# Performance work log

Measured on AMD Instinct MI355X. Metric: run time of the kernel, lower is better.

The kernel has to match this reference:

```python
import jax, jax.numpy as jnp
import numpy as np

N, E, B = 20000, 100000, 16
U_SZ, U_RED = 4096, 256
EDGE_H, EDGE_OUT = 1024, 512
NODE_H = 512
X_DIM, EA_DIM = 9, 1


def _lin(key, fan_out, fan_in):
    kw, kb = jax.random.split(key)
    s = 1.0 / np.sqrt(fan_in)
    w = jax.random.uniform(kw, (fan_out, fan_in), jnp.float32, -s, s)
    b = jax.random.uniform(kb, (fan_out,), jnp.float32, -s, s)
    return w, b


def setup_inputs() -> dict:
    key = jax.random.key(0)
    ks = jax.random.split(key, 16)
    inp = {}
    inp["x"] = jax.random.normal(ks[0], (N, X_DIM), jnp.float32)
    inp["edge_index"] = jax.random.randint(ks[1], (2, E), 0, N, jnp.int64)
    inp["edge_attr"] = jax.random.normal(ks[2], (E, EA_DIM), jnp.float32)
    inp["u"] = jax.random.normal(ks[3], (B, U_SZ), jnp.float32)
    inp["batch"] = jnp.sort(jax.random.randint(ks[4], (N,), 0, B, jnp.int64))
    # select_dim_reduction: Linear(4096, 256)
    inp["w_sel"], inp["b_sel"] = _lin(ks[5], U_RED, U_SZ)
    # edge MLP: 275 -> 1024 -> 1024 -> 1024 -> 1024 -> 512
    e_in = EA_DIM + 2 * X_DIM + U_RED  # 275
    inp["ew0"], inp["eb0"] = _lin(ks[6], EDGE_H, e_in)
    inp["ew1"], inp["eb1"] = _lin(ks[7], EDGE_H, EDGE_H)
    inp["ew2"], inp["eb2"] = _lin(ks[8], EDGE_H, EDGE_H)
    inp["ew3"], inp["eb3"] = _lin(ks[9], EDGE_H, EDGE_H)
    inp["ew4"], inp["eb4"] = _lin(ks[10], EDGE_OUT, EDGE_H)
    # node_mlp_1: (9+512) -> 512 -> 512 (relu after each)
    inp["nw0"], inp["nb0"] = _lin(ks[11], NODE_H, X_DIM + EDGE_OUT)
    inp["nw1"], inp["nb1"] = _lin(ks[12], NODE_H, NODE_H)
    # node_mlp_2: (9+512+256) -> 512 -> 1
    inp["mw0"], inp["mb0"] = _lin(ks[13], NODE_H, X_DIM + NODE_H + U_RED)
    inp["mw1"], inp["mb1"] = _lin(ks[14], 1, NODE_H)
    return inp


def reference(x, edge_index, edge_attr, u, batch,
              w_sel, b_sel,
              ew0, eb0, ew1, eb1, ew2, eb2, ew3, eb3, ew4, eb4,
              nw0, nb0, nw1, nb1, mw0, mb0, mw1, mb1):
    row, col = edge_index[0], edge_index[1]
    u_r = u @ w_sel.T + b_sel                       # [B, 256]
    eb_idx = batch[row]                             # edge -> graph
    # EdgeModel: cat([src, dest, edge_attr, u[batch]]) -> MLP
    e_in = jnp.concatenate([x[row], x[col], edge_attr, u_r[eb_idx]], axis=1)  # [E,275]
    h = jax.nn.relu(e_in @ ew0.T + eb0)
    h = jax.nn.relu(h @ ew1.T + eb1)
    h = jax.nn.relu(h @ ew2.T + eb2)
    h = jax.nn.relu(h @ ew3.T + eb3)
    edge_out = h @ ew4.T + eb4                      # [E, 512]
    # NodeModel: gather x[col], edge MLP, scatter_mean onto row
    n_in = jnp.concatenate([x[col], edge_out], axis=1)  # [E, 521]
    h = jax.nn.relu(n_in @ nw0.T + nb0)
    h = jax.nn.relu(h @ nw1.T + nb1)                # [E, 512]
    seg_sum = jax.ops.segment_sum(h, row, num_segments=x.shape[0])
    cnt = jax.ops.segment_sum(jnp.ones((h.shape[0],), h.dtype), row, num_segments=x.shape[0])
    agg = seg_sum / jnp.maximum(cnt, 1.0)[:, None]  # scatter_mean
    m_in = jnp.concatenate([x, agg, u_r[batch]], axis=1)  # [N, 777]
    h2 = jax.nn.relu(m_in @ mw0.T + mb0)
    out = h2 @ mw1.T + mb1                          # [N, 1]
    return jnp.squeeze(out)
```

## Files before the change

kernel.cpp:

```cpp
#include <hip/hip_runtime.h>


#define NN 20000
#define EE 100000
#define BB 16

typedef _Float16 f16x8 __attribute__((ext_vector_type(8)));
typedef _Float16 f16x4 __attribute__((ext_vector_type(4)));
typedef float f32x4 __attribute__((ext_vector_type(4)));

__device__ __forceinline__ int clampi(int v, int hi) {
    return v < 0 ? 0 : (v >= hi ? hi - 1 : v);
}

__device__ __forceinline__ void gld_lds16(const void* g, void* l) {
    __builtin_amdgcn_global_load_lds(
        (const __attribute__((address_space(1))) unsigned int*)g,
        (__attribute__((address_space(3))) unsigned int*)l, 16, 0, 0);
}

template <int MODE>
__global__ __launch_bounds__(256, 4) void gemm_blk(
    const _Float16* __restrict__ A,
    const _Float16* __restrict__ Wt,
    int KT, int KTs,
    const float* __restrict__ bias, int ldbias, const int* __restrict__ gbid,
    void* __restrict__ C, int KTo, int ktOff,
    int ldc,
    const int* __restrict__ srow, float* __restrict__ aux,
    int M, int relu)
{
    __shared__ char smem[32768];
    _Float16* As = (_Float16*)smem;
    _Float16* Bs = As + 8192;

    const int tid  = threadIdx.x;
    const int lane = tid & 63;
    const int wid  = tid >> 6;
    const int wm = (wid & 1) << 6;
    const int wn = (wid >> 1) << 6;

    const int nb = gridDim.x;
    const int MT = gridDim.y;
    int f = blockIdx.y * nb + blockIdx.x;
    const int MT8 = MT & ~7;
    int p, c;
    if (f < MT8 * nb) {
        c = (f >> 3) % nb;
        p = (f & 7) + 8 * ((f >> 3) / nb);
    } else {
        int g = f - MT8 * nb;
        p = MT8 + g / nb;
        c = g % nb;
    }

    f32x4 acc[4][4];
#pragma unroll
    for (int i = 0; i < 4; ++i)
#pragma unroll
        for (int j = 0; j < 4; ++j) acc[i][j] = (f32x4){0.f, 0.f, 0.f, 0.f};

    const _Float16* pA = A + (size_t)p * KTs * 4096;
    const _Float16* pB = Wt + (size_t)c * KT * 4096;
    const int cb0 = wid * 64;
    const int cb1 = 256 + wid * 64;
    const int kq  = (lane >> 4) * 128;
    const int l15 = lane & 15;
    const int l4  = (lane >> 4) << 2;

    int kt = 0;
    for (; kt + 2 <= KT; kt += 2) {
        __syncthreads();
        gld_lds16(pA + (size_t)(cb0 + lane) * 8,        As + cb0 * 8);
        gld_lds16(pA + (size_t)(cb1 + lane) * 8,        As + cb1 * 8);
        gld_lds16(pA + 4096 + (size_t)(cb0 + lane) * 8, As + 4096 + cb0 * 8);
        gld_lds16(pA + 4096 + (size_t)(cb1 + lane) * 8, As + 4096 + cb1 * 8);
        gld_lds16(pB + (size_t)(cb0 + lane) * 8,        Bs + cb0 * 8);
        gld_lds16(pB + (size_t)(cb1 + lane) * 8,        Bs + cb1 * 8);
        gld_lds16(pB + 4096 + (size_t)(cb0 + lane) * 8, Bs + 4096 + cb0 * 8);
        gld_lds16(pB + 4096 + (size_t)(cb1 + lane) * 8, Bs + 4096 + cb1 * 8);
        pA += 8192; pB += 8192;
        __syncthreads();

#pragma unroll
        for (int s = 0; s < 2; ++s) {
            f16x8 af[4], bf[4];
            const int sb = s * 4096;
#pragma unroll
            for (int i = 0; i < 4; ++i)
                af[i] = *(const f16x8*)(As + sb + (size_t)((kq + wm + i * 16 + l15) << 3));
#pragma unroll
            for (int j = 0; j < 4; ++j)
                bf[j] = *(const f16x8*)(Bs + sb + (size_t)((kq + wn + j * 16 + l15) << 3));
#pragma unroll
            for (int i = 0; i < 4; ++i)
#pragma unroll
                for (int j = 0; j < 4; ++j)
                    acc[i][j] = __builtin_amdgcn_mfma_f32_16x16x32_f16(af[i], bf[j], acc[i][j], 0, 0, 0);
        }
    }
    if (kt < KT) {
        __syncthreads();
        gld_lds16(pA + (size_t)(cb0 + lane) * 8, As + cb0 * 8);
        gld_lds16(pA + (size_t)(cb1 + lane) * 8, As + cb1 * 8);
        gld_lds16(pB + (size_t)(cb0 + lane) * 8, Bs + cb0 * 8);
        gld_lds16(pB + (size_t)(cb1 + lane) * 8, Bs + cb1 * 8);
        __syncthreads();
        f16x8 af[4], bf[4];
#pragma unroll
        for (int i = 0; i < 4; ++i)
            af[i] = *(const f16x8*)(As + (size_t)((kq + wm + i * 16 + l15) << 3));
#pragma unroll
        for (int j = 0; j < 4; ++j)
            bf[j] = *(const f16x8*)(Bs + (size_t)((kq + wn + j * 16 + l15) << 3));
#pragma unroll
        for (int i = 0; i < 4; ++i)
#pragma unroll
            for (int j = 0; j < 4; ++j)
                acc[i][j] = __builtin_amdgcn_mfma_f32_16x16x32_f16(af[i], bf[j], acc[i][j], 0, 0, 0);
    }

    if (MODE == 0) {
        _Float16* tr = (_Float16*)smem;
#pragma unroll
        for (int pass = 0; pass < 2; ++pass) {
            __syncthreads();
            if (wm == pass * 64) {
#pragma unroll
                for (int i = 0; i < 4; ++i) {
#pragma unroll
                    for (int v = 0; v < 4; ++v) {
                        const int lr = i * 16 + l4 + v;
                        const float* brow = bias;
                        if (gbid) {
                            int m = p * 128 + pass * 64 + lr;
                            if (m >= M) m = M - 1;
                            brow = bias + (size_t)clampi(gbid[m], BB) * ldbias;
                        }
#pragma unroll
                        for (int j = 0; j < 4; ++j) {
                            const int cc = wn + j * 16 + l15;
                            float val = acc[i][j][v] + brow[c * 128 + cc];
                            if (relu) val = fmaxf(val, 0.f);
                            tr[lr * 132 + cc] = (_Float16)val;
                        }
                    }
                }
            }
            __syncthreads();
#pragma unroll
            for (int it = 0; it < 4; ++it) {
                const int id = it * 256 + tid;
                const int r  = id & 63;
                const int cg = id >> 6;
                f16x4 lo = *(const f16x4*)(tr + r * 132 + cg * 8);
                f16x4 hi = *(const f16x4*)(tr + r * 132 + cg * 8 + 4);
                f16x8 v8;
#pragma unroll
                for (int t = 0; t < 4; ++t) { v8[t] = lo[t]; v8[t + 4] = hi[t]; }
                const int kti = ktOff + (c << 2) + (cg >> 2);
                const int gr  = pass * 64 + r;
                size_t o = (((size_t)p * KTo + kti) * 4 + (cg & 3)) * 1024 + (size_t)gr * 8;
                *(f16x8*)((_Float16*)C + o) = v8;
            }
        }
    } else if (MODE == 1) {
#pragma unroll
        for (int i = 0; i < 4; ++i) {
#pragma unroll
            for (int v = 0; v < 4; ++v) {
                const int m = p * 128 + wm + i * 16 + l4 + v;
                if (m >= M) continue;
                const float* brow = bias;
                if (gbid) brow = bias + (size_t)clampi(gbid[m], BB) * ldbias;
#pragma unroll
                for (int j = 0; j < 4; ++j) {
                    const int col = c * 128 + wn + j * 16 + l15;
                    float val = acc[i][j][v] + brow[col];
                    if (relu) val = fmaxf(val, 0.f);
                    ((float*)C)[(size_t)m * ldc + col] = val;
                }
            }
        }
    } else if (MODE == 2) {
        float* trf = (float*)smem;
#pragma unroll
        for (int pass = 0; pass < 4; ++pass) {
            __syncthreads();
            if (wm == ((pass >> 1) << 6)) {
                const int i0 = (pass & 1) << 1;
#pragma unroll
                for (int ii = 0; ii < 2; ++ii) {
                    const int i = i0 + ii;
                    const int lr = ii * 16 + l4;
#pragma unroll
                    for (int v = 0; v < 4; ++v) {
#pragma unroll
                        for (int j = 0; j < 4; ++j) {
                            const int cc = wn + j * 16 + l15;
                            float val = acc[i][j][v] + bias[c * 128 + cc];
                            if (relu) val = fmaxf(val, 0.f);
                            trf[(lr + v) * 130 + cc] = val;
                        }
                    }
                }
            }
            __syncthreads();
            const int ebase = p * 128 + pass * 32;
#pragma unroll
            for (int it = 0; it < 16; ++it) {
                const int id = it * 256 + tid;
                const int lr = id >> 7;
                const int colg = id & 127;
                const int el = ebase + lr;
                if (el < M) {
                    const int node = clampi(srow[el], NN);
                    atomicAdd(&aux[(size_t)node * 512 + c * 128 + colg],
                              trf[lr * 130 + colg]);
                }
            }
        }
    } else {
        const float* mw1 = aux;
        float* out = (float*)C;
#pragma unroll
        for (int i = 0; i < 4; ++i) {
#pragma unroll
            for (int v = 0; v < 4; ++v) {
                const int m = p * 128 + wm + i * 16 + l4 + v;
                const int mc = m < M ? m : M - 1;
                const float* brow = bias + (size_t)clampi(gbid[mc], BB) * ldbias;
                float s = 0.f;
#pragma unroll
                for (int j = 0; j < 4; ++j) {
                    const int col = c * 128 + wn + j * 16 + l15;
                    float val = acc[i][j][v] + brow[col];
                    val = fmaxf(val, 0.f);
                    s += val * mw1[col];
                }
                s += __shfl_down(s, 8, 16);
                s += __shfl_down(s, 4, 16);
                s += __shfl_down(s, 2, 16);
                s += __shfl_down(s, 1, 16);
                if (l15 == 0 && m < M) atomicAdd(&out[m], s);
            }
        }
    }
}


__global__ void k_w2h_blk(const float* __restrict__ src, _Float16* __restrict__ dst,
                          int N, int Ksrc, int Kd, int mode)
{
    int t = blockIdx.x * blockDim.x + threadIdx.x;
    if (t >= N * Kd) return;
    int n = t / Kd, k = t - n * Kd;
    float v = 0.f;
    if (mode == 0)      { if (k < Ksrc) v = src[(size_t)n * Ksrc + k]; }
    else if (mode == 1) { if (k < 19) v = src[(size_t)n * 275 + k]; }
    else if (mode == 2) { if (k < 9) v = src[(size_t)n * Ksrc + k];
                          else if (k >= 32 && k < 544) v = src[(size_t)n * Ksrc + 9 + (k - 32)]; }
    else if (mode == 4) { if (k < Ksrc) v = src[(size_t)k * N + n]; }
    else                { v = src[(size_t)n * Ksrc + 9 + k]; }
    int KT = Kd >> 5;
    int nt = n >> 7, r = n & 127, kt = k >> 5, kg = (k >> 3) & 3, ko = k & 7;
    dst[(((size_t)nt * KT + kt) * 4 + kg) * 1024 + (size_t)r * 8 + ko] = (_Float16)v;
}

__global__ void k_fill_w32(const float* __restrict__ nw0, _Float16* __restrict__ whnc)
{
    int t = blockIdx.x * blockDim.x + threadIdx.x;
    if (t >= 512 * 32) return;
    int n = t >> 5, k = t & 31;
    float v = (k < 9) ? nw0[(size_t)n * 521 + k] : 0.f;
    int nt = n >> 7, r = n & 127, kg = (k >> 3) & 3, ko = k & 7;
    whnc[(((size_t)nt * 33 + 32) * 4 + kg) * 1024 + (size_t)r * 8 + ko] = (_Float16)v;
}

__global__ void k_bfuse(const float* __restrict__ nw0, const float* __restrict__ eb4,
                        const float* __restrict__ nb0, float* __restrict__ bf)
{
    int wave = (blockIdx.x * 256 + threadIdx.x) >> 6;
    int lane = threadIdx.x & 63;
    if (wave >= 512) return;
    const float* wr = nw0 + (size_t)wave * 521 + 9;
    float s = 0.f;
#pragma unroll
    for (int i = 0; i < 8; ++i) s += wr[lane * 8 + i] * eb4[lane * 8 + i];
    for (int off = 32; off; off >>= 1) s += __shfl_down(s, off);
    if (lane == 0) bf[wave] = s + nb0[wave];
}

__global__ void k_u_r(const float* __restrict__ u, const float* __restrict__ w_sel,
                      const float* __restrict__ b_sel, float* __restrict__ u_r)
{
    int wave = (blockIdx.x * 256 + threadIdx.x) >> 6;
    int lane = threadIdx.x & 63;
    int b = wave >> 8, n = wave & 255;
    const float4* u4 = (const float4*)(u + (size_t)b * 4096);
    const float4* w4 = (const float4*)(w_sel + (size_t)n * 4096);
    float s = 0.f;
    for (int i = lane; i < 1024; i += 64) {
        float4 a = u4[i], c = w4[i];
        s += a.x * c.x + a.y * c.y + a.z * c.z + a.w * c.w;
    }
    for (int off = 32; off; off >>= 1) s += __shfl_down(s, off);
    if (lane == 0) u_r[b * 256 + n] = s + b_sel[n];
}

__global__ void k_graph_bias(const float* __restrict__ u_r, const float* __restrict__ w,
                             const float* __restrict__ b, float* __restrict__ ub,
                             int Nout, int Ksrc, int koff)
{
    int wave = (blockIdx.x * 256 + threadIdx.x) >> 6;
    int lane = threadIdx.x & 63;
    if (wave >= 16 * Nout) return;
    int g = wave / Nout, n = wave - g * Nout;
    const float* ur = u_r + (size_t)g * 256;
    const float* wr = w + (size_t)n * Ksrc + koff;
    float s = 0.f;
#pragma unroll
    for (int i = 0; i < 4; ++i) s += ur[lane * 4 + i] * wr[lane * 4 + i];
    for (int off = 32; off; off >>= 1) s += __shfl_down(s, off);
    if (lane == 0) ub[(size_t)g * Nout + n] = s + b[n];
}

__global__ void k_gbe(const int* __restrict__ row, const int* __restrict__ batch,
                      int* __restrict__ gbe, float* __restrict__ cnt)
{
    int e = blockIdx.x * blockDim.x + threadIdx.x;
    if (e >= EE) return;
    int r = clampi(row[e], NN);
    gbe[e] = clampi(batch[r], BB);
    atomicAdd(&cnt[r], 1.f);
}

__global__ void k_init_out(float* __restrict__ out, const float* __restrict__ mb1)
{
    int t = blockIdx.x * blockDim.x + threadIdx.x;
    if (t < NN) out[t] = mb1[0];
}

__global__ void k_gather_edge_blk(const float* __restrict__ x, const float* __restrict__ ea,
                                  const int* __restrict__ row, const int* __restrict__ col,
                                  _Float16* __restrict__ dst, _Float16* __restrict__ pong,
                                  int e0, int ec, int MTR)
{
    int t = blockIdx.x * blockDim.x + threadIdx.x;
    if (t >= MTR * 4) return;
    int r = t >> 2, kg = t & 3;
    int e = e0 + r; int emax = e0 + ec - 1;
    if (e > emax) e = emax;
    int ri = clampi(row[e], NN), ci = clampi(col[e], NN);
    f16x8 v;
    f16x8 vx = (f16x8)(_Float16)0.f;
#pragma unroll
    for (int j = 0; j < 8; ++j) {
        int cc = kg * 8 + j;
        float fv = 0.f;
        if (cc < 9)       fv = x[(size_t)ri * 9 + cc];
        else if (cc < 18) fv = x[(size_t)ci * 9 + (cc - 9)];
        else if (cc == 18) fv = ea[e];
        v[j] = (_Float16)fv;
        if (cc < 9) vx[j] = (_Float16)x[(size_t)ci * 9 + cc];
    }
    *(f16x8*)(dst + (size_t)(r >> 7) * 4096 + (size_t)kg * 1024 + (size_t)(r & 127) * 8) = v;
    *(f16x8*)(pong + (((size_t)(r >> 7) * 33 + 32) * 4 + kg) * 1024 + (size_t)(r & 127) * 8) = vx;
}

__global__ void k_gather_min(const float* __restrict__ x, const float* __restrict__ agg,
                             const float* __restrict__ cnt, _Float16* __restrict__ dst, int MTR)
{
    int t = blockIdx.x * blockDim.x + threadIdx.x;
    if (t >= MTR * 68) return;
    int r = t / 68, q = t - r * 68;
    int kt = q >> 2, kg = q & 3;
    int n = r < NN ? r : NN - 1;
    f16x8 v = (f16x8)(_Float16)0.f;
    if (kt == 0) {
#pragma unroll
        for (int j = 0; j < 8; ++j) {
            int cc = kg * 8 + j;
            if (cc < 9) v[j] = (_Float16)x[(size_t)n * 9 + cc];
        }
    } else {
        float inv = 1.f / fmaxf(cnt[n], 1.f);
        int cbase = (kt - 1) * 32 + kg * 8;
        const float4* ap = (const float4*)(agg + (size_t)n * 512 + cbase);
        float4 a0 = ap[0], a1 = ap[1];
        v[0] = (_Float16)(a0.x * inv); v[1] = (_Float16)(a0.y * inv);
        v[2] = (_Float16)(a0.z * inv); v[3] = (_Float16)(a0.w * inv);
        v[4] = (_Float16)(a1.x * inv); v[5] = (_Float16)(a1.y * inv);
        v[6] = (_Float16)(a1.z * inv); v[7] = (_Float16)(a1.w * inv);
    }
    *(f16x8*)(dst + ((size_t)(r >> 7) * 17 + kt) * 4096 + (size_t)kg * 1024 + (size_t)(r & 127) * 8) = v;
}


#define GRID1(n) dim3(((n) + 255) / 256)

static inline void gemmB0(hipStream_t s, const _Float16* A, const _Float16* Wt, int KT, int KTs,
                          const float* bias, int ldbias, const int* gbid,
                          void* C, int KTo, int ktOff,
                          int M, int MT, int NT, int relu)
{
    hipLaunchKernelGGL(gemm_blk<0>, dim3(NT, MT), dim3(256), 0, s,
                       A, Wt, KT, KTs, bias, ldbias, gbid, C, KTo, ktOff, 0,
                       nullptr, nullptr, M, relu);
}
static inline void gemmB2(hipStream_t s, const _Float16* A, const _Float16* Wt, int KT, int KTs,
                          const float* bias, const int* srow, float* agg,
                          int M, int MT, int NT, int relu)
{
    hipLaunchKernelGGL(gemm_blk<2>, dim3(NT, MT), dim3(256), 0, s,
                       A, Wt, KT, KTs, bias, 0, nullptr, nullptr, 0, 0, 0,
                       srow, agg, M, relu);
}
static inline void gemmB3(hipStream_t s, const _Float16* A, const _Float16* Wt, int KT, int KTs,
                          const float* bias, int ldbias, const int* gbid,
                          float* out, const float* mw1,
                          int M, int MT, int NT)
{
    hipLaunchKernelGGL(gemm_blk<3>, dim3(NT, MT), dim3(256), 0, s,
                       A, Wt, KT, KTs, bias, ldbias, gbid, out, 0, 0, 0,
                       nullptr, (float*)mw1, M, 1);
}

extern "C" void kernel_launch(void* const* d_in, const int* in_sizes, int n_in,
                              void* d_out, int out_size, void* d_ws, size_t ws_size,
                              hipStream_t stream)
{
    const float* x     = (const float*)d_in[0];
    const int*   ei    = (const int*)d_in[1];
    const float* ea    = (const float*)d_in[2];
    const float* u     = (const float*)d_in[3];
    const int*   batch = (const int*)d_in[4];
    const float* w_sel = (const float*)d_in[5];
    const float* b_sel = (const float*)d_in[6];
    const float* ew0 = (const float*)d_in[7];   const float* eb0 = (const float*)d_in[8];
    const float* ew1 = (const float*)d_in[9];   const float* eb1 = (const float*)d_in[10];
    const float* ew2 = (const float*)d_in[11];  const float* eb2 = (const float*)d_in[12];
    const float* ew3 = (const float*)d_in[13];  const float* eb3 = (const float*)d_in[14];
    const float* ew4 = (const float*)d_in[15];  const float* eb4 = (const float*)d_in[16];
    const float* nw0 = (const float*)d_in[17];  const float* nb0 = (const float*)d_in[18];
    const float* nw1 = (const float*)d_in[19];  const float* nb1 = (const float*)d_in[20];
    const float* mw0 = (const float*)d_in[21];  const float* mb0 = (const float*)d_in[22];
    const float* mw1 = (const float*)d_in[23];  const float* mb1 = (const float*)d_in[24];

    const int* row = ei;
    const int* col = ei + EE;

    char* W = (char*)d_ws;
    size_t off = 0;
    auto alloc = [&](size_t bytes) -> char* {
        char* p = W + off;
        off = (off + bytes + 255) & ~(size_t)255;
        return p;
    };
    float*    cnt   = (float*)alloc(20000 * 4);
    float*    agg   = (float*)alloc((size_t)NN * 512 * 4);
    float*    zbias = (float*)alloc(1024 * 4);
    const size_t zeroBytes = off;
    float*    u_r  = (float*)alloc(16 * 256 * 4);
    float*    ub0  = (float*)alloc(16 * 1024 * 4);
    float*    ubm  = (float*)alloc(16 * 512 * 4);
    float*    bfu  = (float*)alloc(512 * 4);
    int*      gbe  = (int*)alloc((size_t)EE * 4);
    _Float16* wh0   = (_Float16*)alloc((size_t)8 * 1 * 4096 * 2);
    _Float16* wh1   = (_Float16*)alloc((size_t)8 * 32 * 4096 * 2);
    _Float16* wh2   = (_Float16*)alloc((size_t)8 * 32 * 4096 * 2);
    _Float16* wh3   = (_Float16*)alloc((size_t)8 * 32 * 4096 * 2);
    _Float16* whnc  = (_Float16*)alloc((size_t)4 * 33 * 4096 * 2);
    _Float16* whn1  = (_Float16*)alloc((size_t)4 * 16 * 4096 * 2);
    _Float16* whm0  = (_Float16*)alloc((size_t)4 * 17 * 4096 * 2);
    _Float16* nw0eoB= (_Float16*)alloc((size_t)4 * 16 * 4096 * 2);
    _Float16* ew4T  = (_Float16*)alloc((size_t)8 * 16 * 4096 * 2);
    const int MTm = (NN + 127) / 128;
    _Float16* m_in = (_Float16*)alloc((size_t)MTm * 17 * 4096 * 2);
    const size_t fixedBytes = off;

    static const int ecOpts[] = {50000, 25000, 12500, 10000, 5000};
    int EC = 5000;
    for (int i = 0; i < 5; ++i) {
        int ec = ecOpts[i];
        size_t MTRc = (size_t)((ec + 127) / 128) * 128;
        size_t need = fixedBytes + MTRc * 64 + 2 * (MTRc * 2112) + 4096;
        if (need <= ws_size) { EC = ec; break; }
    }
    const int MT  = (EC + 127) / 128;
    const size_t MTR = (size_t)MT * 128;
    _Float16* e_in = (_Float16*)alloc(MTR * 64);
    _Float16* ping = (_Float16*)alloc(MTR * 2112);
    _Float16* pong = (_Float16*)alloc(MTR * 2112);
    const int NCH = (EE + EC - 1) / EC;

    (void)hipMemsetAsync(W, 0, zeroBytes, stream);
    hipLaunchKernelGGL(k_init_out, GRID1(NN), dim3(256), 0, stream, (float*)d_out, mb1);

    hipLaunchKernelGGL(k_u_r, dim3(1024), dim3(256), 0, stream, u, w_sel, b_sel, u_r);
    hipLaunchKernelGGL(k_graph_bias, GRID1(16 * 1024 * 64), dim3(256), 0, stream,
                       u_r, ew0, eb0, ub0, 1024, 275, 19);
    hipLaunchKernelGGL(k_graph_bias, GRID1(16 * 512 * 64), dim3(256), 0, stream,
                       u_r, mw0, mb0, ubm, 512, 777, 521);
    hipLaunchKernelGGL(k_gbe, GRID1(EE), dim3(256), 0, stream, row, batch, gbe, cnt);
    hipLaunchKernelGGL(k_bfuse, dim3(128), dim3(256), 0, stream, nw0, eb4, nb0, bfu);

    auto pack = [&](const float* w, _Float16* wh, int N, int Ksrc, int Kd, int mode) {
        hipLaunchKernelGGL(k_w2h_blk, GRID1(N * Kd), dim3(256), 0, stream, w, wh, N, Ksrc, Kd, mode);
    };
    pack(ew0, wh0, 1024, 275, 32, 1);
    pack(ew1, wh1, 1024, 1024, 1024, 0);
    pack(ew2, wh2, 1024, 1024, 1024, 0);
    pack(ew3, wh3, 1024, 1024, 1024, 0);
    pack(nw1, whn1, 512, 512, 512, 0);
    pack(mw0, whm0, 512, 777, 544, 2);
    pack(nw0, nw0eoB, 512, 521, 512, 5);
    pack(ew4, ew4T, 1024, 512, 512, 4);
    gemmB0(stream, nw0eoB, ew4T, 16, 16, zbias, 0, nullptr, whnc, 33, 0, 512, 4, 8, 0);
    hipLaunchKernelGGL(k_fill_w32, GRID1(512 * 32), dim3(256), 0, stream, nw0, whnc);

    for (int ch = 0; ch < NCH; ++ch) {
        int e0 = ch * EC;
        int ec = EC; if (e0 + ec > EE) ec = EE - e0;
        hipLaunchKernelGGL(k_gather_edge_blk, GRID1((int)MTR * 4), dim3(256), 0, stream,
                           x, ea, row, col, e_in, pong, e0, ec, (int)MTR);
        gemmB0(stream, e_in, wh0, 1, 1, ub0, 1024, gbe + e0, ping, 33, 0, ec, MT, 8, 1);
        gemmB0(stream, ping, wh1, 32, 33, eb1, 0, nullptr, pong, 33, 0, ec, MT, 8, 1);
        gemmB0(stream, pong, wh2, 32, 33, eb2, 0, nullptr, ping, 33, 0, ec, MT, 8, 1);
        gemmB0(stream, ping, wh3, 32, 33, eb3, 0, nullptr, pong, 33, 0, ec, MT, 8, 1);
        gemmB0(stream, pong, whnc, 33, 33, bfu, 0, nullptr, ping, 16, 0, ec, MT, 4, 1);
        gemmB2(stream, ping, whn1, 16, 16, nb1, row + e0, agg, ec, MT, 4, 1);
    }

    hipLaunchKernelGGL(k_gather_min, GRID1((int)(MTm * 128) * 68), dim3(256), 0, stream,
                       x, agg, cnt, m_in, MTm * 128);
    gemmB3(stream, m_in, whm0, 17, 17, ubm, 512, batch, (float*)d_out, mw1, NN, MTm, 4);
}
```

Measured before the change: 1.501 ms.

## Add 256x256-tile double-buffered GEMM kernel for the three 1024x1024 edge layers

Adds a new gemm256 kernel with 512 threads per block, 256x256 output tiles, 128 KB of LDS double buffering via global_load_lds, interleaved MFMA and staging with priority hints, and an LDS-transposed fp16 epilogue. It replaces the three hidden 1024x1024 edge-MLP layers, and the chunk row padding is rounded up to 256. Larger tiles raise arithmetic intensity and data reuse per block. The cost is lower occupancy and a tile count that may not divide evenly across CUs.

New measurement: 1.524 ms. No clear change (+1.5%).

```diff
diff --git a/kernel.cpp b/kernel.cpp
--- a/kernel.cpp
+++ b/kernel.cpp
@@ -17,6 +17,146 @@
     __builtin_amdgcn_global_load_lds(
         (const __attribute__((address_space(1))) unsigned int*)g,
         (__attribute__((address_space(3))) unsigned int*)l, 16, 0, 0);
+}
+
+__global__ __launch_bounds__(512, 2) void gemm256(
+    const _Float16* __restrict__ Ag, const _Float16* __restrict__ Wt,
+    int KT, int KTs, const float* __restrict__ bias,
+    _Float16* __restrict__ C, int KTo, int ktOff)
+{
+    __shared__ _Float16 As[32768];
+    __shared__ _Float16 Bs[32768];
+
+    const int tid  = threadIdx.x;
+    const int lane = tid & 63;
+    const int wid  = tid >> 6;
+    const int wm = wid & 1;
+    const int wn = wid >> 1;
+    const int l15 = lane & 15;
+    const int l4  = (lane >> 4) << 2;
+
+    const int nb = gridDim.x;
+    const int MT2 = gridDim.y;
+    int f = blockIdx.y * nb + blockIdx.x;
+    const int MT8 = MT2 & ~7;
+    int p, c;
+    if (f < MT8 * nb) {
+        c = (f >> 3) % nb;
+        p = (f & 7) + 8 * ((f >> 3) / nb);
+    } else {
+        int g = f - MT8 * nb;
+        p = MT8 + g / nb;
+        c = g % nb;
+    }
+
+    const int KTT = KT >> 1;
+    const size_t soff = (size_t)tid * 8;
+    const int doff = (tid & ~63) * 8;
+    const int aoff = wm * 4096 + ((lane >> 4) << 10) + l15 * 8;
+    const int boff = (wn >> 1) * 4096 + ((lane >> 4) << 10)
+                   + ((wn & 1) * 64 + l15) * 8;
+
+    auto stageA = [&](int tn, int s) {
+        const size_t kk = (size_t)(2 * tn + s);
+        const _Float16* g0 = Ag + ((size_t)(2 * p)     * KTs + kk) * 4096 + soff;
+        const _Float16* g1 = Ag + ((size_t)(2 * p + 1) * KTs + kk) * 4096 + soff;
+        _Float16* d = As + ((tn & 1) << 14) + (s << 13) + doff;
+        gld_lds16(g0, d);
+        gld_lds16(g1, d + 4096);
+    };
+    auto stageB = [&](int tn, int s) {
+        const size_t kk = (size_t)(2 * tn + s);
+        const _Float16* g0 = Wt + ((size_t)(2 * c)     * KT + kk) * 4096 + soff;
+        const _Float16* g1 = Wt + ((size_t)(2 * c + 1) * KT + kk) * 4096 + soff;
+        _Float16* d = Bs + ((tn & 1) << 14) + (s << 13) + doff;
+        gld_lds16(g0, d);
+        gld_lds16(g1, d + 4096);
+    };
+
+    f32x4 acc[8][4];
+#pragma unroll
+    for (int i = 0; i < 8; ++i)
+#pragma unroll
+        for (int j = 0; j < 4; ++j) acc[i][j] = (f32x4){0.f, 0.f, 0.f, 0.f};
+
+    stageA(0, 0); stageB(0, 0); stageA(0, 1); stageB(0, 1);
+
+    for (int t = 0; t < KTT; ++t) {
+        const int pb = (t & 1) << 14;
+#pragma unroll
+        for (int sub = 0; sub < 2; ++sub) {
+            if (t == KTT - 1 && sub == 1)
+                asm volatile("s_waitcnt vmcnt(0)" ::: "memory");
+            else
+                asm volatile("s_waitcnt vmcnt(4)" ::: "memory");
+            __builtin_amdgcn_s_barrier();
+            const _Float16* Asub = As + pb + (sub << 13) + aoff;
+            const _Float16* Bsub = Bs + pb + (sub << 13) + boff;
+            f16x8 af[4], bf[4];
+#pragma unroll
+            for (int j = 0; j < 4; ++j) bf[j] = *(const f16x8*)(Bsub + j * 128);
+#pragma unroll
+            for (int i = 0; i < 4; ++i) af[i] = *(const f16x8*)(Asub + i * 128);
+            if (t + 1 < KTT) stageA(t + 1, sub);
+            __builtin_amdgcn_s_setprio(1);
+#pragma unroll
+            for (int i = 0; i < 4; ++i)
+#pragma unroll
+                for (int j = 0; j < 4; ++j)
+                    acc[i][j] = __builtin_amdgcn_mfma_f32_16x16x32_f16(
+                        af[i], bf[j], acc[i][j], 0, 0, 0);
+            __builtin_amdgcn_s_setprio(0);
+            __builtin_amdgcn_s_barrier();
+#pragma unroll
+            for (int i = 0; i < 4; ++i)
+                af[i] = *(const f16x8*)(Asub + (4 + i) * 128);
+            if (t + 1 < KTT) stageB(t + 1, sub);
+            __builtin_amdgcn_s_setprio(1);
+#pragma unroll
+            for (int i = 0; i < 4; ++i)
+#pragma unroll
+                for (int j = 0; j < 4; ++j)
+                    acc[4 + i][j] = __builtin_amdgcn_mfma_f32_16x16x32_f16(
+                        af[i], bf[j], acc[4 + i][j], 0, 0, 0);
+            __builtin_amdgcn_s_setprio(0);
+        }
+    }
+
+    _Float16* tr = As;
+#pragma unroll
+    for (int pass = 0; pass < 4; ++pass) {
+        __syncthreads();
+        if (wm == (pass >> 1)) {
+            const int fi = (pass & 1) << 2;
+#pragma unroll
+            for (int i = 0; i < 4; ++i) {
+#pragma unroll
+                for (int v = 0; v < 4; ++v) {
+                    const int lr = i * 16 + l4 + v;
+#pragma unroll
+                    for (int j = 0; j < 4; ++j) {
+                        const int cc = wn * 64 + j * 16 + l15;
+                        float val = acc[fi + i][j][v] + bias[c * 256 + cc];
+                        val = fmaxf(val, 0.f);
+                        tr[lr * 264 + cc] = (_Float16)val;
+                    }
+                }
+            }
+        }
+        __syncthreads();
+#pragma unroll
+        for (int it = 0; it < 4; ++it) {
+            const int id = it * 512 + tid;
+            const int r  = id & 63;
+            const int cg = id >> 6;
+            f16x8 v8 = *(const f16x8*)(tr + r * 264 + cg * 8);
+            const int kt = ktOff + c * 8 + (cg >> 2);
+            const int mt_out = 2 * p + (pass >> 1);
+            const int r128 = ((pass & 1) << 6) + r;
+            *(f16x8*)(C + (((size_t)mt_out * KTo + kt) * 4 + (cg & 3)) * 1024
+                        + (size_t)r128 * 8) = v8;
+        }
+    }
 }
 
 template <int MODE>
@@ -483,12 +623,13 @@
     int EC = 5000;
     for (int i = 0; i < 5; ++i) {
         int ec = ecOpts[i];
-        size_t MTRc = (size_t)((ec + 127) / 128) * 128;
+        size_t MTRc = (size_t)((ec + 255) / 256) * 256;
         size_t need = fixedBytes + MTRc * 64 + 2 * (MTRc * 2112) + 4096;
         if (need <= ws_size) { EC = ec; break; }
     }
-    const int MT  = (EC + 127) / 128;
-    const size_t MTR = (size_t)MT * 128;
+    const size_t MTR = (size_t)((EC + 255) / 256) * 256;
+    const int MT  = (int)(MTR / 128);
+    const int MT2 = (int)(MTR / 256);
     _Float16* e_in = (_Float16*)alloc(MTR * 64);
     _Float16* ping = (_Float16*)alloc(MTR * 2112);
     _Float16* pong = (_Float16*)alloc(MTR * 2112);
@@ -525,9 +666,12 @@
         hipLaunchKernelGGL(k_gather_edge_blk, GRID1((int)MTR * 4), dim3(256), 0, stream,
                            x, ea, row, col, e_in, pong, e0, ec, (int)MTR);
         gemmB0(stream, e_in, wh0, 1, 1, ub0, 1024, gbe + e0, ping, 33, 0, ec, MT, 8, 1);
-        gemmB0(stream, ping, wh1, 32, 33, eb1, 0, nullptr, pong, 33, 0, ec, MT, 8, 1);
-        gemmB0(stream, pong, wh2, 32, 33, eb2, 0, nullptr, ping, 33, 0, ec, MT, 8, 1);
-        gemmB0(stream, ping, wh3, 32, 33, eb3, 0, nullptr, pong, 33, 0, ec, MT, 8, 1);
+        hipLaunchKernelGGL(gemm256, dim3(4, MT2), dim3(512), 0, stream,
+                           ping, wh1, 32, 33, eb1, pong, 33, 0);
+        hipLaunchKernelGGL(gemm256, dim3(4, MT2), dim3(512), 0, stream,
+                           pong, wh2, 32, 33, eb2, ping, 33, 0);
+        hipLaunchKernelGGL(gemm256, dim3(4, MT2), dim3(512), 0, stream,
+                           ping, wh3, 32, 33, eb3, pong, 33, 0);
         gemmB0(stream, pong, whnc, 33, 33, bfu, 0, nullptr, ping, 16, 0, ec, MT, 4, 1);
         gemmB2(stream, ping, whn1, 16, 16, nb1, row + e0, agg, ec, MT, 4, 1);
     }
```
